# Optimization experiments

Measured on AMD Instinct MI355X. Metric: run time of the kernel, lower is better.

Reference implementation:

```python
import jax, jax.numpy as jnp
import numpy as np

N_NODES = 100000
N_EDGES = 640000
F_DIM = 128   # node_feature_dim
D_DIM = 128   # state_dim
ROUNDS = 4


def setup_inputs() -> dict:
    key = jax.random.key(0)
    ks = jax.random.split(key, 8)
    s = 1.0 / np.sqrt(D_DIM)
    return {
        "x": jax.random.normal(ks[0], (N_NODES, F_DIM), dtype=jnp.float32),
        "edge_index": jax.random.randint(ks[1], (2, N_EDGES), 0, N_NODES, dtype=jnp.int64),
        "Wi": jax.random.normal(ks[2], (F_DIM, D_DIM), dtype=jnp.float32) * s,
        "bi": jax.random.normal(ks[3], (D_DIM,), dtype=jnp.float32) * s,
        "Wm": jax.random.normal(ks[4], (ROUNDS, D_DIM, D_DIM), dtype=jnp.float32) * s,
        "bm": jax.random.normal(ks[5], (ROUNDS, D_DIM), dtype=jnp.float32) * s,
        "Wu": jax.random.normal(ks[6], (ROUNDS, D_DIM, D_DIM), dtype=jnp.float32) * s,
        "bu": jax.random.normal(ks[7], (ROUNDS, D_DIM), dtype=jnp.float32) * s,
    }


def reference(x, edge_index, Wi, bi, Wm, bm, Wu, bu):
    num_nodes = x.shape[0]
    src = edge_index[0]  # from-node (messages are gathered from here)
    dst = edge_index[1]  # to-node (scatter-add target)

    # input_net: Linear + ReLU
    state = jax.nn.relu(x @ Wi + bi)  # (N, D)

    def step(state, params):
        Wm_r, bm_r, Wu_r, bu_r = params
        message = jax.nn.relu(state @ Wm_r + bm_r)          # (N, D)
        gathered = message[src]                              # (E, D) gather
        aggregated = jax.ops.segment_sum(gathered, dst,
                                         num_segments=num_nodes)  # scatter-add
        return state + jax.nn.relu(aggregated @ Wu_r + bu_r), None

    state, _ = jax.lax.scan(step, state, (Wm, bm, Wu, bu))
    # original: zeros(state_dim) + state broadcasts to (N, D)
    return state
```

## Files before the change

kernel.cpp:

```cpp
#include <hip/hip_runtime.h>

#define NN 100000
#define NE 640000
#define DD 128
#define ROUNDS 4
#define CAP 32
#define NFT 3125
#define PREPB 768
#define BUILDB 256
#define FG 768
#define KPH 136

typedef float f32x4 __attribute__((ext_vector_type(4)));
typedef float f32x2 __attribute__((ext_vector_type(2)));
typedef _Float16 half8 __attribute__((ext_vector_type(8)));

__device__ inline unsigned char to_fp8(float v) {
    return (unsigned char)(__builtin_amdgcn_cvt_pk_fp8_f32(v, 0.f, 0, 0) & 0xff);
}

__global__ __launch_bounds__(128) void wprep_k(
    const float* __restrict__ Wi, const float* __restrict__ Wm,
    const float* __restrict__ Wu, _Float16* __restrict__ WT)
{
    const int mat = blockIdx.x >> 7;
    const int k   = blockIdx.x & 127;
    const int n   = threadIdx.x;
    const float* W = (mat == 0) ? Wi
                   : (mat <= 4) ? Wm + (size_t)(mat - 1) * DD * DD
                                : Wu + (size_t)(mat - 5) * DD * DD;
    WT[(size_t)mat * DD * DD + (size_t)n * DD + k] = (_Float16)W[(size_t)k * DD + n];
}

__global__ __launch_bounds__(256, 3) void prep_k(
    const float* __restrict__ x,
    const _Float16* __restrict__ WiT, const _Float16* __restrict__ Wm0T,
    const float* __restrict__ bi, const float* __restrict__ bm0,
    _Float16* __restrict__ Sh, unsigned char* __restrict__ msg0,
    const int* __restrict__ src, const int* __restrict__ dst,
    int* __restrict__ cursor, int* __restrict__ bucket)
{
    if (blockIdx.x < BUILDB) {
        for (int e = blockIdx.x * 256 + threadIdx.x; e < NE; e += BUILDB * 256) {
            const int d = dst[e];
            const int s = src[e];
            const int pos = atomicAdd(&cursor[d], 1);
            if (pos < CAP) bucket[(long long)d * CAP + pos] = s;
        }
        return;
    }

    __shared__ _Float16 Ash[32 * KPH];

    const int tid  = threadIdx.x;
    const int lane = tid & 63;
    const int wave = tid >> 6;
    const int ln   = lane & 15;
    const int q    = lane >> 4;
    const int colBase = wave * 32;

    half8 WI[4][2], WM[4][2];
#pragma unroll
    for (int s = 0; s < 4; s++)
#pragma unroll
        for (int b = 0; b < 2; b++) {
            const size_t off = (size_t)(colBase + b * 16 + ln) * DD + s * 32 + q * 8;
            WI[s][b] = *(const half8*)&WiT[off];
            WM[s][b] = *(const half8*)&Wm0T[off];
        }
    float biasi[2], biasm[2];
#pragma unroll
    for (int b = 0; b < 2; b++) {
        biasi[b] = bi[colBase + b * 16 + ln];
        biasm[b] = bm0[colBase + b * 16 + ln];
    }

    const int grow = tid >> 3;
    const int grp  = tid & 7;
    const int gcol = grp * 16;

    for (int tileB = blockIdx.x - BUILDB; tileB < NFT; tileB += PREPB - BUILDB) {
        const float* xr = x + ((size_t)tileB * 32 + grow) * DD + gcol;
        const float4 f0 = *(const float4*)&xr[0];
        const float4 f1 = *(const float4*)&xr[4];
        const float4 f2 = *(const float4*)&xr[8];
        const float4 f3 = *(const float4*)&xr[12];
        half8 hx0, hx1;
        hx0[0] = (_Float16)f0.x; hx0[1] = (_Float16)f0.y;
        hx0[2] = (_Float16)f0.z; hx0[3] = (_Float16)f0.w;
        hx0[4] = (_Float16)f1.x; hx0[5] = (_Float16)f1.y;
        hx0[6] = (_Float16)f1.z; hx0[7] = (_Float16)f1.w;
        hx1[0] = (_Float16)f2.x; hx1[1] = (_Float16)f2.y;
        hx1[2] = (_Float16)f2.z; hx1[3] = (_Float16)f2.w;
        hx1[4] = (_Float16)f3.x; hx1[5] = (_Float16)f3.y;
        hx1[6] = (_Float16)f3.z; hx1[7] = (_Float16)f3.w;

        __syncthreads();
        *(half8*)&Ash[grow * KPH + gcol]     = hx0;
        *(half8*)&Ash[grow * KPH + gcol + 8] = hx1;
        __syncthreads();

        f32x4 acc[2][2];
#pragma unroll
        for (int h = 0; h < 2; h++)
#pragma unroll
            for (int b = 0; b < 2; b++)
                acc[h][b] = (f32x4){biasi[b], biasi[b], biasi[b], biasi[b]};
#pragma unroll
        for (int s = 0; s < 4; s++) {
            const half8 a0 = *(const half8*)&Ash[(ln)      * KPH + s * 32 + q * 8];
            const half8 a1 = *(const half8*)&Ash[(16 + ln) * KPH + s * 32 + q * 8];
#pragma unroll
            for (int b = 0; b < 2; b++) {
                acc[0][b] = __builtin_amdgcn_mfma_f32_16x16x32_f16(a0, WI[s][b], acc[0][b], 0, 0, 0);
                acc[1][b] = __builtin_amdgcn_mfma_f32_16x16x32_f16(a1, WI[s][b], acc[1][b], 0, 0, 0);
            }
        }
        __syncthreads();

#pragma unroll
        for (int h = 0; h < 2; h++)
#pragma unroll
            for (int b = 0; b < 2; b++) {
                const int col = colBase + b * 16 + ln;
#pragma unroll
                for (int r = 0; r < 4; r++) {
                    const int lrow = h * 16 + q * 4 + r;
                    const size_t row = (size_t)tileB * 32 + lrow;
                    const _Float16 v = (_Float16)fmaxf(acc[h][b][r], 0.f);
                    Sh[row * DD + col] = v;
                    Ash[lrow * KPH + col] = v;
                }
            }
        __syncthreads();

        f32x4 acc2[2][2];
#pragma unroll
        for (int h = 0; h < 2; h++)
#pragma unroll
            for (int b = 0; b < 2; b++)
                acc2[h][b] = (f32x4){biasm[b], biasm[b], biasm[b], biasm[b]};
#pragma unroll
        for (int s = 0; s < 4; s++) {
            const half8 a0 = *(const half8*)&Ash[(ln)      * KPH + s * 32 + q * 8];
            const half8 a1 = *(const half8*)&Ash[(16 + ln) * KPH + s * 32 + q * 8];
#pragma unroll
            for (int b = 0; b < 2; b++) {
                acc2[0][b] = __builtin_amdgcn_mfma_f32_16x16x32_f16(a0, WM[s][b], acc2[0][b], 0, 0, 0);
                acc2[1][b] = __builtin_amdgcn_mfma_f32_16x16x32_f16(a1, WM[s][b], acc2[1][b], 0, 0, 0);
            }
        }
#pragma unroll
        for (int h = 0; h < 2; h++)
#pragma unroll
            for (int b = 0; b < 2; b++) {
                const int col = colBase + b * 16 + ln;
#pragma unroll
                for (int r = 0; r < 4; r++) {
                    const size_t row = (size_t)tileB * 32 + h * 16 + q * 4 + r;
                    msg0[row * DD + col] = to_fp8(fmaxf(acc2[h][b][r], 0.f));
                }
            }
    }
}

__global__ __launch_bounds__(256, 3) void fused_round_k(
    const unsigned char* __restrict__ msgIn,
    const int* __restrict__ cursor,
    const int* __restrict__ bucket,
    const _Float16* __restrict__ WuT, const float* __restrict__ bu_r,
    const _Float16* __restrict__ WmT, const float* __restrict__ bm_r,
    const _Float16* __restrict__ Rh,
    _Float16* __restrict__ ShOut,
    unsigned char* __restrict__ msgOut,
    float* __restrict__ Of)
{
    __shared__ _Float16 Ash[32 * KPH];

    const int tid  = threadIdx.x;
    const int lane = tid & 63;
    const int wave = tid >> 6;
    const int ln   = lane & 15;
    const int q    = lane >> 4;
    const int colBase = wave * 32;

    half8 WU[4][2], WM[4][2];
#pragma unroll
    for (int s = 0; s < 4; s++)
#pragma unroll
        for (int b = 0; b < 2; b++) {
            const size_t off = (size_t)(colBase + b * 16 + ln) * DD + s * 32 + q * 8;
            WU[s][b] = *(const half8*)&WuT[off];
            if (WmT) WM[s][b] = *(const half8*)&WmT[off];
        }
    float biasu[2], biasm[2];
#pragma unroll
    for (int b = 0; b < 2; b++) {
        biasu[b] = bu_r[colBase + b * 16 + ln];
        biasm[b] = WmT ? bm_r[colBase + b * 16 + ln] : 0.f;
    }

    const int grow = tid >> 3;
    const int grp  = tid & 7;
    const int gcol = grp * 16;

    int cnt = 0;
    int idxr[4];
#pragma unroll
    for (int i = 0; i < 4; i++) idxr[i] = 0;
    {
        const int node = blockIdx.x * 32 + grow;
        cnt = cursor[node];
        const int ibase = node * CAP;
#pragma unroll
        for (int i = 0; i < 4; i++) idxr[i] = bucket[ibase + grp + 8 * i];
    }

    for (int tileB = blockIdx.x; tileB < NFT; tileB += gridDim.x) {
        const int nextT = tileB + gridDim.x;
        int cntN = 0;
        int idxrN[4];
#pragma unroll
        for (int i = 0; i < 4; i++) idxrN[i] = 0;
        if (nextT < NFT) {
            const int nodeN = nextT * 32 + grow;
            cntN = cursor[nodeN];
            const int ibaseN = nodeN * CAP;
#pragma unroll
            for (int i = 0; i < 4; i++) idxrN[i] = bucket[ibaseN + grp + 8 * i];
        }

        int c = cnt;
        if (c > CAP) c = CAP;

        float a[16];
#pragma unroll
        for (int i = 0; i < 16; i++) a[i] = 0.f;

        for (int j = 0; j < c; j += 4) {
            int ix[4];
#pragma unroll
            for (int u = 0; u < 4; u++) {
                const int jj = (j + u) & 31;
                int v = __shfl(idxr[jj >> 3], (lane & 56) | (jj & 7), 64);
                ix[u] = ((unsigned)v < NN) ? v : 0;
            }
            int4 v[4];
#pragma unroll
            for (int u = 0; u < 4; u++)
                v[u] = *(const int4*)&msgIn[(size_t)ix[u] * DD + gcol];
#pragma unroll
            for (int u = 0; u < 4; u++) {
                if (j + u < c) {
                    const int4 t = v[u];
                    const f32x2 p0 = __builtin_amdgcn_cvt_pk_f32_fp8(t.x, 0);
                    const f32x2 p1 = __builtin_amdgcn_cvt_pk_f32_fp8(t.x, 1);
                    const f32x2 p2 = __builtin_amdgcn_cvt_pk_f32_fp8(t.y, 0);
                    const f32x2 p3 = __builtin_amdgcn_cvt_pk_f32_fp8(t.y, 1);
                    const f32x2 p4 = __builtin_amdgcn_cvt_pk_f32_fp8(t.z, 0);
                    const f32x2 p5 = __builtin_amdgcn_cvt_pk_f32_fp8(t.z, 1);
                    const f32x2 p6 = __builtin_amdgcn_cvt_pk_f32_fp8(t.w, 0);
                    const f32x2 p7 = __builtin_amdgcn_cvt_pk_f32_fp8(t.w, 1);
                    a[0]  += p0.x; a[1]  += p0.y; a[2]  += p1.x; a[3]  += p1.y;
                    a[4]  += p2.x; a[5]  += p2.y; a[6]  += p3.x; a[7]  += p3.y;
                    a[8]  += p4.x; a[9]  += p4.y; a[10] += p5.x; a[11] += p5.y;
                    a[12] += p6.x; a[13] += p6.y; a[14] += p7.x; a[15] += p7.y;
                }
            }
        }

        half8 h0, h1;
#pragma unroll
        for (int i = 0; i < 8; i++) { h0[i] = (_Float16)a[i]; h1[i] = (_Float16)a[8 + i]; }

        __syncthreads();
        *(half8*)&Ash[grow * KPH + gcol]     = h0;
        *(half8*)&Ash[grow * KPH + gcol + 8] = h1;
        __syncthreads();

        _Float16 rh[2][2][4];
#pragma unroll
        for (int h = 0; h < 2; h++)
#pragma unroll
            for (int b = 0; b < 2; b++)
#pragma unroll
                for (int r = 0; r < 4; r++) {
                    const size_t row = (size_t)tileB * 32 + h * 16 + q * 4 + r;
                    rh[h][b][r] = Rh[row * DD + colBase + b * 16 + ln];
                }

        f32x4 acc[2][2];
#pragma unroll
        for (int h = 0; h < 2; h++)
#pragma unroll
            for (int b = 0; b < 2; b++)
                acc[h][b] = (f32x4){biasu[b], biasu[b], biasu[b], biasu[b]};
#pragma unroll
        for (int s = 0; s < 4; s++) {
            const half8 a0 = *(const half8*)&Ash[(ln)      * KPH + s * 32 + q * 8];
            const half8 a1 = *(const half8*)&Ash[(16 + ln) * KPH + s * 32 + q * 8];
#pragma unroll
            for (int b = 0; b < 2; b++) {
                acc[0][b] = __builtin_amdgcn_mfma_f32_16x16x32_f16(a0, WU[s][b], acc[0][b], 0, 0, 0);
                acc[1][b] = __builtin_amdgcn_mfma_f32_16x16x32_f16(a1, WU[s][b], acc[1][b], 0, 0, 0);
            }
        }

        if (!WmT) {
#pragma unroll
            for (int h = 0; h < 2; h++)
#pragma unroll
                for (int b = 0; b < 2; b++) {
                    const int col = colBase + b * 16 + ln;
#pragma unroll
                    for (int r = 0; r < 4; r++) {
                        const size_t row = (size_t)tileB * 32 + h * 16 + q * 4 + r;
                        Of[row * DD + col] = fmaxf(acc[h][b][r], 0.f) + (float)rh[h][b][r];
                    }
                }
            cnt = cntN;
#pragma unroll
            for (int i = 0; i < 4; i++) idxr[i] = idxrN[i];
            continue;
        }

        __syncthreads();
#pragma unroll
        for (int h = 0; h < 2; h++)
#pragma unroll
            for (int b = 0; b < 2; b++) {
                const int col = colBase + b * 16 + ln;
#pragma unroll
                for (int r = 0; r < 4; r++) {
                    const int lrow = h * 16 + q * 4 + r;
                    const size_t row = (size_t)tileB * 32 + lrow;
                    const _Float16 v =
                        (_Float16)(fmaxf(acc[h][b][r], 0.f) + (float)rh[h][b][r]);
                    ShOut[row * DD + col] = v;
                    Ash[lrow * KPH + col] = v;
                }
            }
        __syncthreads();

        f32x4 acc2[2][2];
#pragma unroll
        for (int h = 0; h < 2; h++)
#pragma unroll
            for (int b = 0; b < 2; b++)
                acc2[h][b] = (f32x4){biasm[b], biasm[b], biasm[b], biasm[b]};
#pragma unroll
        for (int s = 0; s < 4; s++) {
            const half8 a0 = *(const half8*)&Ash[(ln)      * KPH + s * 32 + q * 8];
            const half8 a1 = *(const half8*)&Ash[(16 + ln) * KPH + s * 32 + q * 8];
#pragma unroll
            for (int b = 0; b < 2; b++) {
                acc2[0][b] = __builtin_amdgcn_mfma_f32_16x16x32_f16(a0, WM[s][b], acc2[0][b], 0, 0, 0);
                acc2[1][b] = __builtin_amdgcn_mfma_f32_16x16x32_f16(a1, WM[s][b], acc2[1][b], 0, 0, 0);
            }
        }
#pragma unroll
        for (int h = 0; h < 2; h++)
#pragma unroll
            for (int b = 0; b < 2; b++) {
                const int col = colBase + b * 16 + ln;
#pragma unroll
                for (int r = 0; r < 4; r++) {
                    const size_t row = (size_t)tileB * 32 + h * 16 + q * 4 + r;
                    msgOut[row * DD + col] = to_fp8(fmaxf(acc2[h][b][r], 0.f));
                }
            }

        cnt = cntN;
#pragma unroll
        for (int i = 0; i < 4; i++) idxr[i] = idxrN[i];
    }
}

extern "C" void kernel_launch(void* const* d_in, const int* in_sizes, int n_in,
                              void* d_out, int out_size, void* d_ws, size_t ws_size,
                              hipStream_t stream) {
    const float* x  = (const float*)d_in[0];
    const int*   ei = (const int*)d_in[1];
    const float* Wi = (const float*)d_in[2];
    const float* bi = (const float*)d_in[3];
    const float* Wm = (const float*)d_in[4];
    const float* bm = (const float*)d_in[5];
    const float* Wu = (const float*)d_in[6];
    const float* bu = (const float*)d_in[7];

    const int* src = ei;
    const int* dst = ei + NE;

    const size_t NELE = (size_t)NN * DD;
    unsigned char* msgA = (unsigned char*)d_ws;
    unsigned char* msgB = msgA + NELE;
    _Float16* Sh   = (_Float16*)(msgB + NELE);
    _Float16* WT   = Sh + NELE;
    int* cursor = (int*)(WT + 9 * DD * DD);
    int* bucket = cursor + NN;

    hipMemsetAsync(cursor, 0, (size_t)NN * 4, stream);
    hipMemsetAsync(bucket, 0, (size_t)NN * CAP * 4, stream);
    wprep_k<<<9 * 128, 128, 0, stream>>>(Wi, Wm, Wu, WT);

    prep_k<<<PREPB, 256, 0, stream>>>(
        x, WT , WT + 1 * DD * DD , bi, bm,
        Sh, msgA, src, dst, cursor, bucket);

    unsigned char* mIn = msgA;
    unsigned char* mOut = msgB;
    for (int r = 0; r < ROUNDS; r++) {
        const bool last = (r == ROUNDS - 1);
        fused_round_k<<<FG, 256, 0, stream>>>(
            mIn, cursor, bucket,
            WT + (size_t)(5 + r) * DD * DD, bu + (size_t)r * DD,
            last ? nullptr : WT + (size_t)(2 + r) * DD * DD,
            last ? nullptr : bm + (size_t)(r + 1) * DD,
            Sh, Sh, mOut,
            last ? (float*)d_out : nullptr);
        unsigned char* t = mIn; mIn = mOut; mOut = t;
    }
}
```

Before: 308.6 us.

## Prefetch first eight gathered neighbor rows for next tile during GEMM phase

```diff
diff --git a/kernel.cpp b/kernel.cpp
--- a/kernel.cpp
+++ b/kernel.cpp
@@ -8,7 +8,7 @@
 #define NFT 3125
 #define PREPB 768
 #define BUILDB 256
-#define FG 768
+#define FG 512
 #define KPH 136
 
 typedef float f32x4 __attribute__((ext_vector_type(4)));
@@ -164,7 +164,7 @@
     }
 }
 
-__global__ __launch_bounds__(256, 3) void fused_round_k(
+__global__ __launch_bounds__(256, 2) void fused_round_k(
     const unsigned char* __restrict__ msgIn,
     const int* __restrict__ cursor,
     const int* __restrict__ bucket,
@@ -208,12 +208,19 @@
     int idxr[4];
 #pragma unroll
     for (int i = 0; i < 4; i++) idxr[i] = 0;
+    int4 vP[8];
     {
         const int node = blockIdx.x * 32 + grow;
         cnt = cursor[node];
         const int ibase = node * CAP;
 #pragma unroll
         for (int i = 0; i < 4; i++) idxr[i] = bucket[ibase + grp + 8 * i];
+#pragma unroll
+        for (int u = 0; u < 8; u++) {
+            int v = __shfl(idxr[u >> 3], (lane & 56) | (u & 7), 64);
+            const int ix = ((unsigned)v < NN) ? v : 0;
+            vP[u] = *(const int4*)&msgIn[(size_t)ix * DD + gcol];
+        }
     }
 
     for (int tileB = blockIdx.x; tileB < NFT; tileB += gridDim.x) {
@@ -237,7 +244,25 @@
 #pragma unroll
         for (int i = 0; i < 16; i++) a[i] = 0.f;
 
-        for (int j = 0; j < c; j += 4) {
+#pragma unroll
+        for (int u = 0; u < 8; u++) {
+            if (u < c) {
+                const int4 t = vP[u];
+                const f32x2 p0 = __builtin_amdgcn_cvt_pk_f32_fp8(t.x, 0);
+                const f32x2 p1 = __builtin_amdgcn_cvt_pk_f32_fp8(t.x, 1);
+                const f32x2 p2 = __builtin_amdgcn_cvt_pk_f32_fp8(t.y, 0);
+                const f32x2 p3 = __builtin_amdgcn_cvt_pk_f32_fp8(t.y, 1);
+                const f32x2 p4 = __builtin_amdgcn_cvt_pk_f32_fp8(t.z, 0);
+                const f32x2 p5 = __builtin_amdgcn_cvt_pk_f32_fp8(t.z, 1);
+                const f32x2 p6 = __builtin_amdgcn_cvt_pk_f32_fp8(t.w, 0);
+                const f32x2 p7 = __builtin_amdgcn_cvt_pk_f32_fp8(t.w, 1);
+                a[0]  += p0.x; a[1]  += p0.y; a[2]  += p1.x; a[3]  += p1.y;
+                a[4]  += p2.x; a[5]  += p2.y; a[6]  += p3.x; a[7]  += p3.y;
+                a[8]  += p4.x; a[9]  += p4.y; a[10] += p5.x; a[11] += p5.y;
+                a[12] += p6.x; a[13] += p6.y; a[14] += p7.x; a[15] += p7.y;
+            }
+        }
+        for (int j = 8; j < c; j += 4) {
             int ix[4];
 #pragma unroll
             for (int u = 0; u < 4; u++) {
@@ -278,6 +303,15 @@
         *(half8*)&Ash[grow * KPH + gcol + 8] = h1;
         __syncthreads();
 
+        if (nextT < NFT) {
+#pragma unroll
+            for (int u = 0; u < 8; u++) {
+                int v = __shfl(idxrN[u >> 3], (lane & 56) | (u & 7), 64);
+                const int ix = ((unsigned)v < NN) ? v : 0;
+                vP[u] = *(const int4*)&msgIn[(size_t)ix * DD + gcol];
+            }
+        }
+
         _Float16 rh[2][2][4];
 #pragma unroll
         for (int h = 0; h < 2; h++)
```

Result: faster. 293.4 us (-4.9%).

## Prefetch next tile's neighbor messages and double-buffer shared tile to drop barriers

Applied to the files above, without the earlier changes.

```diff
diff --git a/kernel.cpp b/kernel.cpp
--- a/kernel.cpp
+++ b/kernel.cpp
@@ -8,8 +8,9 @@
 #define NFT 3125
 #define PREPB 768
 #define BUILDB 256
-#define FG 768
+#define FG 512
 #define KPH 136
+#define VPN 12
 
 typedef float f32x4 __attribute__((ext_vector_type(4)));
 typedef float f32x2 __attribute__((ext_vector_type(2)));
@@ -17,6 +18,18 @@
 
 __device__ inline unsigned char to_fp8(float v) {
     return (unsigned char)(__builtin_amdgcn_cvt_pk_fp8_f32(v, 0.f, 0, 0) & 0xff);
+}
+
+__device__ inline void acc_fp8x16(const int4 t, float* a) {
+    f32x2 p;
+    p = __builtin_amdgcn_cvt_pk_f32_fp8(t.x, 0); a[0]  += p.x; a[1]  += p.y;
+    p = __builtin_amdgcn_cvt_pk_f32_fp8(t.x, 1); a[2]  += p.x; a[3]  += p.y;
+    p = __builtin_amdgcn_cvt_pk_f32_fp8(t.y, 0); a[4]  += p.x; a[5]  += p.y;
+    p = __builtin_amdgcn_cvt_pk_f32_fp8(t.y, 1); a[6]  += p.x; a[7]  += p.y;
+    p = __builtin_amdgcn_cvt_pk_f32_fp8(t.z, 0); a[8]  += p.x; a[9]  += p.y;
+    p = __builtin_amdgcn_cvt_pk_f32_fp8(t.z, 1); a[10] += p.x; a[11] += p.y;
+    p = __builtin_amdgcn_cvt_pk_f32_fp8(t.w, 0); a[12] += p.x; a[13] += p.y;
+    p = __builtin_amdgcn_cvt_pk_f32_fp8(t.w, 1); a[14] += p.x; a[15] += p.y;
 }
 
 __global__ __launch_bounds__(128) void wprep_k(
@@ -164,7 +177,7 @@
     }
 }
 
-__global__ __launch_bounds__(256, 3) void fused_round_k(
+__global__ __launch_bounds__(256, 2) void fused_round_k(
     const unsigned char* __restrict__ msgIn,
     const int* __restrict__ cursor,
     const int* __restrict__ bucket,
@@ -175,7 +188,7 @@
     unsigned char* __restrict__ msgOut,
     float* __restrict__ Of)
 {
-    __shared__ _Float16 Ash[32 * KPH];
+    __shared__ _Float16 Ash[2][32 * KPH];
 
     const int tid  = threadIdx.x;
     const int lane = tid & 63;
@@ -208,13 +221,22 @@
     int idxr[4];
 #pragma unroll
     for (int i = 0; i < 4; i++) idxr[i] = 0;
+    int4 vP[VPN];
     {
         const int node = blockIdx.x * 32 + grow;
         cnt = cursor[node];
         const int ibase = node * CAP;
 #pragma unroll
         for (int i = 0; i < 4; i++) idxr[i] = bucket[ibase + grp + 8 * i];
-    }
+#pragma unroll
+        for (int u = 0; u < VPN; u++) {
+            int v = __shfl(idxr[u >> 3], (lane & 56) | (u & 7), 64);
+            const int ix = ((unsigned)v < NN) ? v : 0;
+            vP[u] = *(const int4*)&msgIn[(size_t)ix * DD + gcol];
+        }
+    }
+
+    int pp = 0;
 
     for (int tileB = blockIdx.x; tileB < NFT; tileB += gridDim.x) {
         const int nextT = tileB + gridDim.x;
@@ -229,6 +251,16 @@
 #pragma unroll
             for (int i = 0; i < 4; i++) idxrN[i] = bucket[ibaseN + grp + 8 * i];
         }
+        _Float16 rh[2][2][4];
+#pragma unroll
+        for (int h = 0; h < 2; h++)
+#pragma unroll
+            for (int b = 0; b < 2; b++)
+#pragma unroll
+                for (int r = 0; r < 4; r++) {
+                    const size_t row = (size_t)tileB * 32 + h * 16 + q * 4 + r;
+                    rh[h][b][r] = Rh[row * DD + colBase + b * 16 + ln];
+                }
 
         int c = cnt;
         if (c > CAP) c = CAP;
@@ -237,7 +269,11 @@
 #pragma unroll
         for (int i = 0; i < 16; i++) a[i] = 0.f;
 
-        for (int j = 0; j < c; j += 4) {
+#pragma unroll
+        for (int u = 0; u < VPN; u++)
+            if (u < c) acc_fp8x16(vP[u], a);
+
+        for (int j = VPN; j < c; j += 4) {
             int ix[4];
 #pragma unroll
             for (int u = 0; u < 4; u++) {
@@ -250,44 +286,28 @@
             for (int u = 0; u < 4; u++)
                 v[u] = *(const int4*)&msgIn[(size_t)ix[u] * DD + gcol];
 #pragma unroll
-            for (int u = 0; u < 4; u++) {
-                if (j + u < c) {
-                    const int4 t = v[u];
-                    const f32x2 p0 = __builtin_amdgcn_cvt_pk_f32_fp8(t.x, 0);
-                    const f32x2 p1 = __builtin_amdgcn_cvt_pk_f32_fp8(t.x, 1);
-                    const f32x2 p2 = __builtin_amdgcn_cvt_pk_f32_fp8(t.y, 0);
-                    const f32x2 p3 = __builtin_amdgcn_cvt_pk_f32_fp8(t.y, 1);
-                    const f32x2 p4 = __builtin_amdgcn_cvt_pk_f32_fp8(t.z, 0);
-                    const f32x2 p5 = __builtin_amdgcn_cvt_pk_f32_fp8(t.z, 1);
-                    const f32x2 p6 = __builtin_amdgcn_cvt_pk_f32_fp8(t.w, 0);
-                    const f32x2 p7 = __builtin_amdgcn_cvt_pk_f32_fp8(t.w, 1);
-                    a[0]  += p0.x; a[1]  += p0.y; a[2]  += p1.x; a[3]  += p1.y;
-                    a[4]  += p2.x; a[5]  += p2.y; a[6]  += p3.x; a[7]  += p3.y;
-                    a[8]  += p4.x; a[9]  += p4.y; a[10] += p5.x; a[11] += p5.y;
-                    a[12] += p6.x; a[13] += p6.y; a[14] += p7.x; a[15] += p7.y;
-                }
-            }
+            for (int u = 0; u < 4; u++)
+                if (j + u < c) acc_fp8x16(v[u], a);
         }
 
         half8 h0, h1;
 #pragma unroll
         for (int i = 0; i < 8; i++) { h0[i] = (_Float16)a[i]; h1[i] = (_Float16)a[8 + i]; }
 
-        __syncthreads();
-        *(half8*)&Ash[grow * KPH + gcol]     = h0;
-        *(half8*)&Ash[grow * KPH + gcol + 8] = h1;
-        __syncthreads();
-
-        _Float16 rh[2][2][4];
-#pragma unroll
-        for (int h = 0; h < 2; h++)
-#pragma unroll
-            for (int b = 0; b < 2; b++)
-#pragma unroll
-                for (int r = 0; r < 4; r++) {
-                    const size_t row = (size_t)tileB * 32 + h * 16 + q * 4 + r;
-                    rh[h][b][r] = Rh[row * DD + colBase + b * 16 + ln];
-                }
+        const int ab = WmT ? 0 : pp;
+        *(half8*)&Ash[ab][grow * KPH + gcol]     = h0;
+        *(half8*)&Ash[ab][grow * KPH + gcol + 8] = h1;
+
+        if (nextT < NFT) {
+#pragma unroll
+            for (int u = 0; u < VPN; u++) {
+                int v = __shfl(idxrN[u >> 3], (lane & 56) | (u & 7), 64);
+                const int ix = ((unsigned)v < NN) ? v : 0;
+                vP[u] = *(const int4*)&msgIn[(size_t)ix * DD + gcol];
+            }
+        }
+
+        __syncthreads();
 
         f32x4 acc[2][2];
 #pragma unroll
@@ -297,8 +317,8 @@
                 acc[h][b] = (f32x4){biasu[b], biasu[b], biasu[b], biasu[b]};
 #pragma unroll
         for (int s = 0; s < 4; s++) {
-            const half8 a0 = *(const half8*)&Ash[(ln)      * KPH + s * 32 + q * 8];
-            const half8 a1 = *(const half8*)&Ash[(16 + ln) * KPH + s * 32 + q * 8];
+            const half8 a0 = *(const half8*)&Ash[ab][(ln)      * KPH + s * 32 + q * 8];
+            const half8 a1 = *(const half8*)&Ash[ab][(16 + ln) * KPH + s * 32 + q * 8];
 #pragma unroll
             for (int b = 0; b < 2; b++) {
                 acc[0][b] = __builtin_amdgcn_mfma_f32_16x16x32_f16(a0, WU[s][b], acc[0][b], 0, 0, 0);
@@ -318,13 +338,13 @@
                         Of[row * DD + col] = fmaxf(acc[h][b][r], 0.f) + (float)rh[h][b][r];
                     }
                 }
+            pp ^= 1;
             cnt = cntN;
 #pragma unroll
             for (int i = 0; i < 4; i++) idxr[i] = idxrN[i];
             continue;
         }
 
-        __syncthreads();
 #pragma unroll
         for (int h = 0; h < 2; h++)
 #pragma unroll
@@ -337,7 +357,7 @@
                     const _Float16 v =
                         (_Float16)(fmaxf(acc[h][b][r], 0.f) + (float)rh[h][b][r]);
                     ShOut[row * DD + col] = v;
-                    Ash[lrow * KPH + col] = v;
+                    Ash[1][lrow * KPH + col] = v;
                 }
             }
         __syncthreads();
@@ -350,8 +370,8 @@
                 acc2[h][b] = (f32x4){biasm[b], biasm[b], biasm[b], biasm[b]};
 #pragma unroll
         for (int s = 0; s < 4; s++) {
-            const half8 a0 = *(const half8*)&Ash[(ln)      * KPH + s * 32 + q * 8];
-            const half8 a1 = *(const half8*)&Ash[(16 + ln) * KPH + s * 32 + q * 8];
+            const half8 a0 = *(const half8*)&Ash[1][(ln)      * KPH + s * 32 + q * 8];
+            const half8 a1 = *(const half8*)&Ash[1][(16 + ln) * KPH + s * 32 + q * 8];
 #pragma unroll
             for (int b = 0; b < 2; b++) {
                 acc2[0][b] = __builtin_amdgcn_mfma_f32_16x16x32_f16(a0, WM[s][b], acc2[0][b], 0, 0, 0);
```

New measurement: 280.9 us. 1.1x faster.
